# Kernel optimization log

Hardware: AMD Instinct MI355X
Metric: run time of the kernel (lower is better)

## Reference

```python
import jax, jax.numpy as jnp
import numpy as np

SHIFTS = (1, 2, 4, 8)
NL = 8  # num_layer: 8 fixed contrast kernels


def _base_kernels():
    d1 = np.array([[[-1, 0, 0], [0, 1, 0], [0, 0, 0]],
                   [[0, -1, 0], [0, 1, 0], [0, 0, 0]],
                   [[0, 0, -1], [0, 1, 0], [0, 0, 0]],
                   [[0, 0, 0], [0, 1, -1], [0, 0, 0]]], dtype=np.float32).reshape(4, 1, 3, 3)
    d2 = d1[:, :, ::-1, ::-1].copy()
    k = np.concatenate([d1, d2], axis=0)      # [8,1,3,3] fixed contrast kernels
    k0 = k.mean(0, keepdims=True)             # [1,1,3,3] mean kernel (kernel0)
    return jnp.asarray(k), jnp.asarray(k0)


def _depthwise(x, w, dilation):
    # x: [B,C,H,W], w: [C,1,3,3]; torch conv2d(padding='same', groups=C, dilation=d)
    return jax.lax.conv_general_dilated(
        x, w, window_strides=(1, 1), padding='SAME',
        rhs_dilation=(dilation, dilation),
        dimension_numbers=('NCHW', 'OIHW', 'NCHW'),
        feature_group_count=x.shape[1])


def _l2norm(x, eps=1e-12):
    # F.normalize(dim=-1): x / max(||x||_2, eps)
    n = jnp.sqrt(jnp.sum(x * x, axis=-1, keepdims=True))
    return x / jnp.maximum(n, eps)


def setup_inputs() -> dict:
    key = jax.random.key(0)
    ks = jax.random.split(key, 8)
    B, C, H, W = 8, 64, 96, 96
    nh = len(SHIFTS)
    hid = C // nh
    return {
        'cen': jax.random.normal(ks[0], (B, C, H, W), jnp.float32),
        'sum_weights': jax.random.normal(ks[1], (nh, C, 1, 1, 1, 2), jnp.float32),
        'q_w': jax.random.normal(ks[2], (nh, hid, C), jnp.float32) / np.sqrt(C),
        'k_w': jax.random.normal(ks[3], (nh, NL * hid, NL * C), jnp.float32) / np.sqrt(NL * C),
        'v_w': jax.random.normal(ks[4], (nh, NL * hid, NL * C), jnp.float32) / np.sqrt(NL * C),
        'out_w': jax.random.normal(ks[5], (C, C), jnp.float32) / np.sqrt(C),
        'bn_gamma': jnp.ones((C,), jnp.float32),
        'bn_beta': jnp.zeros((C,), jnp.float32),
    }


def reference(cen, sum_weights, q_w, k_w, v_w, out_w, bn_gamma, bn_beta):
    b, c, h, w = cen.shape
    nh = len(SHIFTS)
    K, K0 = _base_kernels()  # [8,1,3,3], [1,1,3,3]

    keys, qrys, vals = [], [], []
    for i, s in enumerate(SHIFTS):
        sw = jax.nn.softmax(sum_weights[i], axis=-1)  # [C,1,1,1,2]
        # mixed kernels: kernel_j*sw0 + kernel0*sw1 per channel -> [8,C,1,3,3]
        mixed = K[:, None] * sw[None, ..., 0] + K0[:, None] * sw[None, ..., 1]
        # 8 depthwise dilated convs, vmapped over the 8 kernels -> [8,B,C,H,W]
        surr = jax.vmap(lambda kw: _depthwise(cen, kw, s))(mixed)
        # torch.cat along channels in kernel-major order (j, c)
        surr = jnp.transpose(surr, (1, 0, 2, 3, 4)).reshape(b, NL * c, h, w)
        keys.append(jnp.einsum('oc,bchw->bohw', k_w[i], surr))
        vals.append(jnp.einsum('oc,bchw->bohw', v_w[i], surr))
        qrys.append(jnp.einsum('oc,bchw->bohw', q_w[i], cen))

    # torch: stack(dim=2).view(b, nh, -1, h*w)  (raw row-major reinterpret)
    keys = jnp.stack(keys, axis=2).reshape(b, nh, -1, h * w)
    qrys = jnp.stack(qrys, axis=2).reshape(b, nh, -1, h * w)
    vals = jnp.stack(vals, axis=2).reshape(b, nh, -1, h * w)

    k_n = _l2norm(keys)  # L2 norm over spatial axis
    q_n = _l2norm(qrys)
    # scores: [b, heads, hid, 8*hid]
    scores = jnp.einsum('bhqs,bhks->bhqk', q_n, k_n) / jnp.sqrt(jnp.float32(h * w))
    # InstanceNorm2d(num_heads), affine=False, eps=1e-5: per (b, head) over (q, k)
    mu = scores.mean(axis=(-2, -1), keepdims=True)
    var = scores.var(axis=(-2, -1), keepdims=True)
    attn = jax.nn.softmax((scores - mu) * jax.lax.rsqrt(var + 1e-5), axis=-1)
    out = jnp.einsum('bhqk,bhks->bhqs', attn, vals).reshape(b, c, h, w)

    # out_conv: 1x1 conv (no bias) + BatchNorm2d (train-mode batch stats) + ReLU
    y = jnp.einsum('oc,bchw->bohw', out_w, out)
    m = y.mean(axis=(0, 2, 3), keepdims=True)
    v2 = y.var(axis=(0, 2, 3), keepdims=True)
    y = (y - m) * jax.lax.rsqrt(v2 + 1e-5)
    y = y * bn_gamma[None, :, None, None] + bn_beta[None, :, None, None]
    return jax.nn.relu(y)
```

## Files before the change

### kernel.cpp

```cpp
#include <hip/hip_runtime.h>
#include <hip/hip_bf16.h>


#define WS_CEN    0UL
#define WS_SPART  12845056UL
#define WS_W      25690112UL
#define WS_Q      28049408UL
#define WS_KV     46923776UL
#define WS_KKP    197918720UL
#define WS_QQP    198213632UL
#define WS_ATTN   198250496UL
#define WS_AB     198512640UL
#define WS_BNP    217387008UL
#define WS_BNF    217681920UL

typedef __attribute__((ext_vector_type(8))) short short8;
typedef __attribute__((ext_vector_type(4))) float f32x4;

__device__ __forceinline__ float bflo(unsigned int u){ return __uint_as_float(u<<16); }
__device__ __forceinline__ float bfhi(unsigned int u){ return __uint_as_float(u & 0xffff0000u); }
__device__ __forceinline__ unsigned short f2bf(float f){
  unsigned int u = __float_as_uint(f);
  return (unsigned short)((u + 0x7fffu + ((u>>16)&1u)) >> 16);
}
__device__ __forceinline__ unsigned short fbits(float f){
  __hip_bfloat16 h = __float2bfloat16(f);
  return __builtin_bit_cast(unsigned short, h);
}

__global__ __launch_bounds__(256) void pad_kernel(const float* __restrict__ cen, unsigned short* __restrict__ cenbf){
  int idx = blockIdx.x*256 + threadIdx.x;
  int px = idx % 112; int t = idx / 112; int py = t % 112; int bc = t / 112;
  int y = py - 8, x = px - 8;
  float v = 0.f;
  if (y >= 0 && y < 96 && x >= 0 && x < 96) v = cen[(size_t)bc*9216 + y*96 + x];
  cenbf[idx] = fbits(v);
}

__global__ __launch_bounds__(256) void prep_kernel(const float* __restrict__ sumw,
    const float* __restrict__ kw, const float* __restrict__ vw, unsigned short* __restrict__ Wb){
  int idx = blockIdx.x*256 + threadIdx.x;
  int o = idx & 255; int r = idx >> 8; int c = r & 63; r >>= 6; int t = r % 9; int i = r / 9;
  float l0 = sumw[(i*64 + c)*2 + 0], l1 = sumw[(i*64 + c)*2 + 1];
  float m = fmaxf(l0, l1);
  float e0 = expf(l0 - m), e1 = expf(l1 - m);
  float inv = 1.f/(e0 + e1);
  float sw0 = e0*inv, sw1 = e1*inv;
  const float* wsrc = (o < 128) ? (kw + ((size_t)i*128 + o)*512 + c)
                                : (vw + ((size_t)i*128 + (o-128))*512 + c);
  float A = 0.f;
  #pragma unroll
  for (int j = 0; j < 8; ++j) A += wsrc[j*64];
  float val;
  if (t == 4) {
    val = A;
  } else {
    const int tmap[9] = {0,1,2,7,0,3,6,5,4};
    int j = tmap[t];
    val = -(wsrc[j*64]*sw0 + A*sw1*0.125f);
  }
  int k = t*64 + c;
  Wb[(((size_t)i*18 + (k>>5))*256 + o)*32 + (k&31)] = f2bf(val);
}

__global__ __launch_bounds__(256) void qproj_kernel(const float* __restrict__ cen,
    const float* __restrict__ qw, unsigned short* __restrict__ qbf){
  __shared__ float WT[64][64];
  int tid = threadIdx.x;
  int st = blockIdx.x, b = blockIdx.y;
  #pragma unroll
  for (int e = 0; e < 16; ++e) {
    int f = e*256 + tid; int c = f >> 6, row = f & 63;
    int i = row & 3, o = row >> 2;
    WT[c][row] = qw[(size_t)i*1024 + o*64 + c];
  }
  __syncthreads();
  int s = st*256 + tid;
  float acc[64];
  #pragma unroll
  for (int r = 0; r < 64; ++r) acc[r] = 0.f;
  const float* cb = cen + (size_t)b*64*9216 + s;
  for (int c = 0; c < 64; ++c) {
    float xv = cb[(size_t)c*9216];
    #pragma unroll
    for (int r4 = 0; r4 < 16; ++r4) {
      float4 w = *(const float4*)&WT[c][r4*4];
      acc[r4*4+0] = fmaf(w.x, xv, acc[r4*4+0]);
      acc[r4*4+1] = fmaf(w.y, xv, acc[r4*4+1]);
      acc[r4*4+2] = fmaf(w.z, xv, acc[r4*4+2]);
      acc[r4*4+3] = fmaf(w.w, xv, acc[r4*4+3]);
    }
  }
  unsigned short* qb = qbf + (size_t)b*64*9216 + s;
  #pragma unroll
  for (int r = 0; r < 64; ++r) qb[(size_t)r*9216] = fbits(acc[r]);
}

__global__ __launch_bounds__(256, 3) void conv_kv_mfma(const unsigned short* __restrict__ cenbf,
    const unsigned short* __restrict__ Wb, unsigned short* __restrict__ KV){
  __shared__ char Xs[2][128*72];
  const int tid = threadIdx.x;
  const int st = blockIdx.x, oc = blockIdx.y, ib = blockIdx.z;
  const int i = ib >> 3, b = ib & 7;
  const int dil = 1 << i;
  const int s0 = st*128;
  const int wave = tid >> 6, lane = tid & 63;
  const int wm = wave >> 1, wn = wave & 1;
  const int l15 = lane & 15, l4 = lane >> 4;
  const int s_idx = tid & 127;
  const int khalf = tid >> 7;
  const int s = s0 + s_idx;
  const int y = s / 96, x = s - y*96;
  const unsigned short* cb = cenbf + (size_t)b*802816 + (size_t)(y+8)*112 + (x+8);

  f32x4 acc[4][4];
  #pragma unroll
  for (int mf = 0; mf < 4; ++mf)
    #pragma unroll
    for (int nf = 0; nf < 4; ++nf)
      acc[mf][nf] = (f32x4){0.f, 0.f, 0.f, 0.f};

  const unsigned short* Wi = Wb + (size_t)i*18*8192;
  const unsigned short* apb = Wi + (size_t)(oc*128 + wm*64 + l15)*32 + l4*8;

  unsigned short vs[16];
  auto gather = [&](int kn){
    int t = kn >> 1;
    int cbase = (kn & 1)*32 + khalf*16;
    int dy = (t/3 - 1)*dil, dx = (t - (t/3)*3 - 1)*dil;
    const unsigned short* p = cb + (size_t)cbase*12544 + (dy*112 + dx);
    #pragma unroll
    for (int j = 0; j < 16; ++j) vs[j] = p[(size_t)j*12544];
  };

  gather(0);
  int buf = 0;
  for (int kc = 0; kc < 18; ++kc) {
    short8 a[4];
    const unsigned short* ap = apb + (size_t)kc*8192;
    #pragma unroll
    for (int mf = 0; mf < 4; ++mf) a[mf] = *(const short8*)(ap + mf*512);
    asm volatile("" ::: "memory");
    char* wp = Xs[buf] + s_idx*72 + khalf*32;
    #pragma unroll
    for (int w = 0; w < 4; ++w) {
      unsigned int p0 = (unsigned int)vs[4*w+0] | ((unsigned int)vs[4*w+1] << 16);
      unsigned int p1 = (unsigned int)vs[4*w+2] | ((unsigned int)vs[4*w+3] << 16);
      *(uint2*)(wp + w*8) = make_uint2(p0, p1);
    }
    if (kc < 17) gather(kc + 1);
    asm volatile("s_waitcnt lgkmcnt(0)" ::: "memory");
    __builtin_amdgcn_s_barrier();
    asm volatile("" ::: "memory");
    short8 bfr[4];
    #pragma unroll
    for (int nf = 0; nf < 4; ++nf) {
      const char* rp = Xs[buf] + (wn*64 + nf*16 + l15)*72 + l4*16;
      uint2 lo = *(const uint2*)rp;
      uint2 hi = *(const uint2*)(rp + 8);
      uint4 tb = make_uint4(lo.x, lo.y, hi.x, hi.y);
      bfr[nf] = *(short8*)&tb;
    }
    #pragma unroll
    for (int mf = 0; mf < 4; ++mf)
      #pragma unroll
      for (int nf = 0; nf < 4; ++nf)
        acc[mf][nf] = __builtin_amdgcn_mfma_f32_16x16x32_bf16(a[mf], bfr[nf], acc[mf][nf], 0, 0, 0);
    buf ^= 1;
  }

  #pragma unroll
  for (int mf = 0; mf < 4; ++mf) {
    #pragma unroll
    for (int nf = 0; nf < 4; ++nf) {
      int scol = s0 + wn*64 + nf*16 + l15;
      int obase = oc*128 + wm*64 + mf*16 + l4*4;
      #pragma unroll
      for (int r = 0; r < 4; ++r)
        KV[((size_t)ib*256 + obase + r)*9216 + scol] = fbits(acc[mf][nf][r]);
    }
  }
}

__global__ __launch_bounds__(256) void scores_mfma(const unsigned short* __restrict__ KV,
    const unsigned short* __restrict__ qbf, float* __restrict__ spart,
    float* __restrict__ kkpart, float* __restrict__ qqpart){
  __shared__ float red[4][2192];
  const int tid = threadIdx.x;
  const int chunk = blockIdx.x, hh = blockIdx.y, b = blockIdx.z;
  const int wave = tid >> 6, lane = tid & 63;
  const int l15 = lane & 15, l4 = lane >> 4;
  const int sbase = chunk*512 + wave*128;

  const unsigned short* qp = qbf + ((size_t)(b*64 + hh*16 + l15))*9216 + sbase + l4*8;
  const unsigned short* kp = KV + ((size_t)(((l15&3)*8 + b)*256 + hh*32 + (l15>>2)))*9216 + sbase + l4*8;

  f32x4 sacc[8], kkacc[8], qqacc;
  #pragma unroll
  for (int nf = 0; nf < 8; ++nf) { sacc[nf] = (f32x4){0,0,0,0}; kkacc[nf] = (f32x4){0,0,0,0}; }
  qqacc = (f32x4){0,0,0,0};

  #pragma unroll
  for (int sl = 0; sl < 4; ++sl) {
    short8 qf = *(const short8*)(qp + sl*32);
    short8 kf[8];
    #pragma unroll
    for (int nf = 0; nf < 8; ++nf) kf[nf] = *(const short8*)(kp + (size_t)nf*36864 + sl*32);
    qqacc = __builtin_amdgcn_mfma_f32_16x16x32_bf16(qf, qf, qqacc, 0, 0, 0);
    #pragma unroll
    for (int nf = 0; nf < 8; ++nf) {
      sacc[nf]  = __builtin_amdgcn_mfma_f32_16x16x32_bf16(qf, kf[nf], sacc[nf], 0, 0, 0);
      kkacc[nf] = __builtin_amdgcn_mfma_f32_16x16x32_bf16(kf[nf], kf[nf], kkacc[nf], 0, 0, 0);
    }
  }
  float* rw = red[wave];
  #pragma unroll
  for (int nf = 0; nf < 8; ++nf)
    #pragma unroll
    for (int r = 0; r < 4; ++r)
      rw[(l4*4 + r)*128 + nf*16 + l15] = sacc[nf][r];
  if ((l15 >> 2) == l4) {
    int r = l15 & 3;
    #pragma unroll
    for (int nf = 0; nf < 8; ++nf) rw[2048 + nf*16 + l15] = kkacc[nf][r];
    rw[2176 + l15] = qqacc[r];
  }
  __syncthreads();
  int pb = (b*4 + hh)*18 + chunk;
  for (int t = tid; t < 2192; t += 256) {
    float v = red[0][t] + red[1][t] + red[2][t] + red[3][t];
    if (t < 2048)       spart[(size_t)pb*2048 + t] = v;
    else if (t < 2176)  kkpart[(size_t)pb*128 + (t - 2048)] = v;
    else                qqpart[(size_t)pb*16 + (t - 2176)] = v;
  }
}

__global__ __launch_bounds__(256) void softmax_kernel(const float* __restrict__ spart,
    const float* __restrict__ kkpart, const float* __restrict__ qqpart, float* __restrict__ attnT){
  const int pb = blockIdx.x, tid = threadIdx.x;
  const int qr = tid >> 4, g = tid & 15;
  __shared__ float kkl[128];
  __shared__ float qql[16];
  __shared__ float red[8];
  __shared__ float stats[2];
  float sv[8] = {0,0,0,0,0,0,0,0};
  for (int ch = 0; ch < 18; ++ch) {
    const float* p = spart + ((size_t)(pb*18 + ch))*2048 + qr*128 + g*8;
    #pragma unroll
    for (int e = 0; e < 8; ++e) sv[e] += p[e];
  }
  if (tid < 128) { float ssum = 0.f; for (int ch = 0; ch < 18; ++ch) ssum += kkpart[(size_t)(pb*18+ch)*128 + tid]; kkl[tid] = ssum; }
  if (tid < 16)  { float ssum = 0.f; for (int ch = 0; ch < 18; ++ch) ssum += qqpart[(size_t)(pb*18+ch)*16 + tid]; qql[tid] = ssum; }
  __syncthreads();
  float qn = fmaxf(sqrtf(qql[qr]), 1e-12f);
  float lsum = 0.f, lsq = 0.f;
  #pragma unroll
  for (int e = 0; e < 8; ++e) {
    float kn = fmaxf(sqrtf(kkl[g*8+e]), 1e-12f);
    float v = sv[e] / (qn * kn * 96.0f);
    sv[e] = v; lsum += v; lsq += v*v;
  }
  #pragma unroll
  for (int m = 1; m <= 32; m <<= 1) { lsum += __shfl_xor(lsum, m); lsq += __shfl_xor(lsq, m); }
  if ((tid & 63) == 0) { red[tid >> 6] = lsum; red[4 + (tid >> 6)] = lsq; }
  __syncthreads();
  if (tid == 0) {
    float ts = red[0]+red[1]+red[2]+red[3];
    float tq = red[4]+red[5]+red[6]+red[7];
    float mean = ts / 2048.0f;
    float var = tq / 2048.0f - mean*mean;
    stats[0] = mean; stats[1] = rsqrtf(var + 1e-5f);
  }
  __syncthreads();
  float mean = stats[0], inv = stats[1];
  float mx = -1e30f;
  #pragma unroll
  for (int e = 0; e < 8; ++e) { sv[e] = (sv[e] - mean) * inv; mx = fmaxf(mx, sv[e]); }
  #pragma unroll
  for (int m = 1; m <= 8; m <<= 1) mx = fmaxf(mx, __shfl_xor(mx, m));
  float es = 0.f;
  #pragma unroll
  for (int e = 0; e < 8; ++e) { sv[e] = expf(sv[e] - mx); es += sv[e]; }
  #pragma unroll
  for (int m = 1; m <= 8; m <<= 1) es += __shfl_xor(es, m);
  float rinv = 1.0f / es;
  #pragma unroll
  for (int e = 0; e < 8; ++e) attnT[(size_t)pb*2048 + (g*8+e)*16 + qr] = sv[e] * rinv;
}

__global__ __launch_bounds__(256) void attnfold_kernel(const float* __restrict__ attnT,
    const float* __restrict__ ow, unsigned short* __restrict__ Ab){
  int idx = blockIdx.x*256 + threadIdx.x;
  int kr = idx & 127, hh = (idx >> 7) & 3, o2 = (idx >> 9) & 63, b = idx >> 15;
  const float* ap = attnT + ((size_t)(b*4 + hh))*2048 + kr*16;
  const float* wp = ow + o2*64 + hh*16;
  float acc = 0.f;
  #pragma unroll
  for (int qr = 0; qr < 16; ++qr) acc += wp[qr] * ap[qr];
  int rc = (kr & 3)*4 + hh, ch = kr >> 2;
  Ab[(((size_t)b*16 + rc)*64 + o2)*32 + ch] = fbits(acc);
}

__global__ __launch_bounds__(256, 3) void ygemm_kernel(const unsigned short* __restrict__ KV,
    const unsigned short* __restrict__ Ab, float* __restrict__ dout, float* __restrict__ bnpart){
  __shared__ char Xs[2][128*72];
  __shared__ float bns[4][32], bnq[4][32];
  const int tid = threadIdx.x;
  const int st = blockIdx.x, b = blockIdx.y;
  const int wave = tid >> 6, lane = tid & 63;
  const int wm = wave >> 1, wn = wave & 1;
  const int l15 = lane & 15, l4 = lane >> 4;
  const int s_idx = tid & 127, khalf = tid >> 7;
  const int s0 = st*128;

  f32x4 acc[2][4];
  #pragma unroll
  for (int mf = 0; mf < 2; ++mf)
    #pragma unroll
    for (int nf = 0; nf < 4; ++nf)
      acc[mf][nf] = (f32x4){0.f, 0.f, 0.f, 0.f};

  const unsigned short* Abb = Ab + ((size_t)b*16*64)*32 + (size_t)(wm*32 + l15)*32 + l4*8;

  unsigned short vs[16];
  auto vgather = [&](int kn){
    int vr = (((kn >> 2)*8 + b)*256 + 128 + (kn & 3)*32) + khalf*16;
    const unsigned short* p = KV + (size_t)vr*9216 + s0 + s_idx;
    #pragma unroll
    for (int j = 0; j < 16; ++j) vs[j] = p[(size_t)j*9216];
  };

  vgather(0);
  int buf = 0;
  for (int kc = 0; kc < 16; ++kc) {
    short8 a[2];
    #pragma unroll
    for (int mf = 0; mf < 2; ++mf) a[mf] = *(const short8*)(Abb + (size_t)kc*2048 + mf*512);
    asm volatile("" ::: "memory");
    char* wp = Xs[buf] + s_idx*72 + khalf*32;
    #pragma unroll
    for (int w = 0; w < 4; ++w) {
      unsigned int p0 = (unsigned int)vs[4*w+0] | ((unsigned int)vs[4*w+1] << 16);
      unsigned int p1 = (unsigned int)vs[4*w+2] | ((unsigned int)vs[4*w+3] << 16);
      *(uint2*)(wp + w*8) = make_uint2(p0, p1);
    }
    if (kc < 15) vgather(kc + 1);
    asm volatile("s_waitcnt lgkmcnt(0)" ::: "memory");
    __builtin_amdgcn_s_barrier();
    asm volatile("" ::: "memory");
    short8 bfr[4];
    #pragma unroll
    for (int nf = 0; nf < 4; ++nf) {
      const char* rp = Xs[buf] + (wn*64 + nf*16 + l15)*72 + l4*16;
      uint2 lo = *(const uint2*)rp;
      uint2 hi = *(const uint2*)(rp + 8);
      uint4 tb = make_uint4(lo.x, lo.y, hi.x, hi.y);
      bfr[nf] = *(short8*)&tb;
    }
    #pragma unroll
    for (int mf = 0; mf < 2; ++mf)
      #pragma unroll
      for (int nf = 0; nf < 4; ++nf)
        acc[mf][nf] = __builtin_amdgcn_mfma_f32_16x16x32_bf16(a[mf], bfr[nf], acc[mf][nf], 0, 0, 0);
    buf ^= 1;
  }

  #pragma unroll
  for (int mf = 0; mf < 2; ++mf) {
    #pragma unroll
    for (int rr = 0; rr < 4; ++rr) {
      int o2 = wm*32 + mf*16 + l4*4 + rr;
      float vsum = 0.f, vsq = 0.f;
      #pragma unroll
      for (int nf = 0; nf < 4; ++nf) {
        float v = acc[mf][nf][rr];
        vsum += v; vsq += v*v;
        dout[((size_t)(b*64 + o2))*9216 + s0 + wn*64 + nf*16 + l15] = v;
      }
      #pragma unroll
      for (int m = 1; m <= 8; m <<= 1) { vsum += __shfl_xor(vsum, m); vsq += __shfl_xor(vsq, m); }
      if (l15 == 0) { bns[wave][mf*16 + l4*4 + rr] = vsum; bnq[wave][mf*16 + l4*4 + rr] = vsq; }
    }
  }
  __syncthreads();
  if (tid < 64) {
    int wmq = tid >> 5, local = tid & 31;
    float s_ = bns[wmq*2][local] + bns[wmq*2+1][local];
    float q_ = bnq[wmq*2][local] + bnq[wmq*2+1][local];
    int bid = b*72 + st;
    bnpart[(size_t)bid*128 + tid] = s_;
    bnpart[(size_t)bid*128 + 64 + tid] = q_;
  }
}

__global__ __launch_bounds__(128) void bncombine_kernel(const float* __restrict__ bnpart, float* __restrict__ bnfin){
  int t = threadIdx.x;
  float a = 0.f;
  for (int blk = 0; blk < 576; ++blk) a += bnpart[(size_t)blk*128 + t];
  bnfin[t] = a;
}

__global__ __launch_bounds__(256) void bnapply_kernel(float* __restrict__ yb,
    const float* __restrict__ bnfin, const float* __restrict__ gamma, const float* __restrict__ beta){
  int gid = blockIdx.x*256 + threadIdx.x;
  int o = (gid / 2304) & 63;
  float mean = bnfin[o] * (1.f/73728.f);
  float var = bnfin[64 + o] * (1.f/73728.f) - mean*mean;
  float inv = rsqrtf(var + 1e-5f);
  float g = gamma[o], be = beta[o];
  float4 v = ((const float4*)yb)[gid];
  v.x = fmaxf((v.x - mean)*inv*g + be, 0.f);
  v.y = fmaxf((v.y - mean)*inv*g + be, 0.f);
  v.z = fmaxf((v.z - mean)*inv*g + be, 0.f);
  v.w = fmaxf((v.w - mean)*inv*g + be, 0.f);
  ((float4*)yb)[gid] = v;
}

extern "C" void kernel_launch(void* const* d_in, const int* in_sizes, int n_in,
                              void* d_out, int out_size, void* d_ws, size_t ws_size,
                              hipStream_t stream) {
  const float* cen   = (const float*)d_in[0];
  const float* sumw  = (const float*)d_in[1];
  const float* qw    = (const float*)d_in[2];
  const float* kw    = (const float*)d_in[3];
  const float* vw    = (const float*)d_in[4];
  const float* ow    = (const float*)d_in[5];
  const float* gamma = (const float*)d_in[6];
  const float* beta  = (const float*)d_in[7];

  char* ws = (char*)d_ws;
  unsigned short* cenbf  = (unsigned short*)(ws + WS_CEN);
  float*          spart  = (float*)(ws + WS_SPART);
  unsigned short* Wb     = (unsigned short*)(ws + WS_W);
  unsigned short* qbf    = (unsigned short*)(ws + WS_Q);
  unsigned short* KV     = (unsigned short*)(ws + WS_KV);
  float*          kkp    = (float*)(ws + WS_KKP);
  float*          qqp    = (float*)(ws + WS_QQP);
  float*          attnT  = (float*)(ws + WS_ATTN);
  unsigned short* Ab     = (unsigned short*)(ws + WS_AB);
  float*          bnp    = (float*)(ws + WS_BNP);
  float*          bnf    = (float*)(ws + WS_BNF);

  pad_kernel     <<<25088, 256, 0, stream>>>(cen, cenbf);
  prep_kernel    <<<2304, 256, 0, stream>>>(sumw, kw, vw, Wb);
  qproj_kernel   <<<dim3(36, 8), 256, 0, stream>>>(cen, qw, qbf);
  conv_kv_mfma   <<<dim3(72, 2, 32), 256, 0, stream>>>(cenbf, Wb, KV);
  scores_mfma    <<<dim3(18, 4, 8), 256, 0, stream>>>(KV, qbf, spart, kkp, qqp);
  softmax_kernel <<<32, 256, 0, stream>>>(spart, kkp, qqp, attnT);
  attnfold_kernel<<<1024, 256, 0, stream>>>(attnT, ow, Ab);
  ygemm_kernel   <<<dim3(72, 8), 256, 0, stream>>>(KV, Ab, (float*)d_out, bnp);
  bncombine_kernel<<<1, 128, 0, stream>>>(bnp, bnf);
  bnapply_kernel <<<4608, 256, 0, stream>>>((float*)d_out, bnf, gamma, beta);
}
```

Before: 427.7 us.

## Enlarge conv_kv tile to full 256 outputs and gather pixel pairs via shifted copy

The dilated-conv MFMA kernel now has each 512-thread block compute all 256 output channels for 256 spatial positions, so the input gather is no longer repeated across two output-channel blocks. Each thread loads two adjacent bf16 pixels with one 32-bit load. To keep those loads aligned for odd horizontal offsets, the pad kernel writes a second copy of the padded input shifted by one element. The weight layout is reorganised per tap with K=64 per step, and the workspace offsets are reshuffled to make room for the extra copy. The costs are more registers per thread (32 accumulator tiles, 16 A fragments), a larger LDS footprint, half as many blocks, and one extra padded-input write.

```diff
diff --git a/kernel.cpp b/kernel.cpp
--- a/kernel.cpp
+++ b/kernel.cpp
@@ -3,16 +3,17 @@
 
 
 #define WS_CEN    0UL
-#define WS_SPART  12845056UL
+#define WS_CEN1   12845056UL
 #define WS_W      25690112UL
 #define WS_Q      28049408UL
 #define WS_KV     46923776UL
-#define WS_KKP    197918720UL
-#define WS_QQP    198213632UL
-#define WS_ATTN   198250496UL
-#define WS_AB     198512640UL
-#define WS_BNP    217387008UL
-#define WS_BNF    217681920UL
+#define WS_SPART  197918720UL
+#define WS_KKP    202637312UL
+#define WS_QQP    202932224UL
+#define WS_ATTN   202969088UL
+#define WS_AB     203231232UL
+#define WS_BNP    203755520UL
+#define WS_BNF    204050432UL
 
 typedef __attribute__((ext_vector_type(8))) short short8;
 typedef __attribute__((ext_vector_type(4))) float f32x4;
@@ -28,13 +29,16 @@
   return __builtin_bit_cast(unsigned short, h);
 }
 
-__global__ __launch_bounds__(256) void pad_kernel(const float* __restrict__ cen, unsigned short* __restrict__ cenbf){
+__global__ __launch_bounds__(256) void pad_kernel(const float* __restrict__ cen,
+    unsigned short* __restrict__ cenbf, unsigned short* __restrict__ cenbf1){
   int idx = blockIdx.x*256 + threadIdx.x;
   int px = idx % 112; int t = idx / 112; int py = t % 112; int bc = t / 112;
   int y = py - 8, x = px - 8;
   float v = 0.f;
   if (y >= 0 && y < 96 && x >= 0 && x < 96) v = cen[(size_t)bc*9216 + y*96 + x];
-  cenbf[idx] = fbits(v);
+  unsigned short h = fbits(v);
+  cenbf[idx] = h;
+  if (idx > 0) cenbf1[idx-1] = h;
 }
 
 __global__ __launch_bounds__(256) void prep_kernel(const float* __restrict__ sumw,
@@ -59,8 +63,7 @@
     int j = tmap[t];
     val = -(wsrc[j*64]*sw0 + A*sw1*0.125f);
   }
-  int k = t*64 + c;
-  Wb[(((size_t)i*18 + (k>>5))*256 + o)*32 + (k&31)] = f2bf(val);
+  Wb[(((size_t)i*9 + t)*256 + o)*64 + c] = f2bf(val);
 }
 
 __global__ __launch_bounds__(256) void qproj_kernel(const float* __restrict__ cen,
@@ -96,85 +99,101 @@
   for (int r = 0; r < 64; ++r) qb[(size_t)r*9216] = fbits(acc[r]);
 }
 
-__global__ __launch_bounds__(256, 3) void conv_kv_mfma(const unsigned short* __restrict__ cenbf,
-    const unsigned short* __restrict__ Wb, unsigned short* __restrict__ KV){
-  __shared__ char Xs[2][128*72];
+__global__ __launch_bounds__(512, 2) void conv_kv_mfma(const unsigned short* __restrict__ cenbf,
+    const unsigned short* __restrict__ cenbf1, const unsigned short* __restrict__ Wb,
+    unsigned short* __restrict__ KV){
+  __shared__ char Xs[2][256*136];
   const int tid = threadIdx.x;
-  const int st = blockIdx.x, oc = blockIdx.y, ib = blockIdx.z;
+  const int st = blockIdx.x, ib = blockIdx.z;
   const int i = ib >> 3, b = ib & 7;
   const int dil = 1 << i;
-  const int s0 = st*128;
+  const int s0 = st*256;
   const int wave = tid >> 6, lane = tid & 63;
-  const int wm = wave >> 1, wn = wave & 1;
+  const int wm = wave >> 2, wn = wave & 3;
   const int l15 = lane & 15, l4 = lane >> 4;
-  const int s_idx = tid & 127;
-  const int khalf = tid >> 7;
-  const int s = s0 + s_idx;
+  const int p = tid & 127, cg = tid >> 7;
+  const int sl = 2*p;
+  const int s = s0 + sl;
   const int y = s / 96, x = s - y*96;
-  const unsigned short* cb = cenbf + (size_t)b*802816 + (size_t)(y+8)*112 + (x+8);
-
-  f32x4 acc[4][4];
-  #pragma unroll
-  for (int mf = 0; mf < 4; ++mf)
+  const long ebase = (long)b*802816 + (long)(cg*16)*12544 + (long)(y+8)*112 + (x+8);
+
+  f32x4 acc[8][4];
+  #pragma unroll
+  for (int mf = 0; mf < 8; ++mf)
     #pragma unroll
     for (int nf = 0; nf < 4; ++nf)
       acc[mf][nf] = (f32x4){0.f, 0.f, 0.f, 0.f};
 
-  const unsigned short* Wi = Wb + (size_t)i*18*8192;
-  const unsigned short* apb = Wi + (size_t)(oc*128 + wm*64 + l15)*32 + l4*8;
-
-  unsigned short vs[16];
-  auto gather = [&](int kn){
-    int t = kn >> 1;
-    int cbase = (kn & 1)*32 + khalf*16;
+  const unsigned short* Wi = Wb + (size_t)i*9*16384;
+  const unsigned short* apb = Wi + (size_t)(wm*128 + l15)*64 + l4*8;
+
+  unsigned int vs[16];
+  auto gather = [&](int t){
     int dy = (t/3 - 1)*dil, dx = (t - (t/3)*3 - 1)*dil;
-    const unsigned short* p = cb + (size_t)cbase*12544 + (dy*112 + dx);
-    #pragma unroll
-    for (int j = 0; j < 16; ++j) vs[j] = p[(size_t)j*12544];
+    long e0 = ebase + dy*112 + dx;
+    const unsigned short* src = (dx & 1) ? (cenbf1 + (e0 - 1)) : (cenbf + e0);
+    #pragma unroll
+    for (int j = 0; j < 16; ++j) vs[j] = *(const unsigned int*)(src + (size_t)j*12544);
   };
 
   gather(0);
   int buf = 0;
-  for (int kc = 0; kc < 18; ++kc) {
-    short8 a[4];
-    const unsigned short* ap = apb + (size_t)kc*8192;
-    #pragma unroll
-    for (int mf = 0; mf < 4; ++mf) a[mf] = *(const short8*)(ap + mf*512);
+  for (int t = 0; t < 9; ++t) {
+    short8 a[8][2];
+    const unsigned short* ap = apb + (size_t)t*16384;
+    #pragma unroll
+    for (int mf = 0; mf < 8; ++mf)
+      #pragma unroll
+      for (int ks = 0; ks < 2; ++ks)
+        a[mf][ks] = *(const short8*)(ap + mf*1024 + ks*32);
     asm volatile("" ::: "memory");
-    char* wp = Xs[buf] + s_idx*72 + khalf*32;
-    #pragma unroll
-    for (int w = 0; w < 4; ++w) {
-      unsigned int p0 = (unsigned int)vs[4*w+0] | ((unsigned int)vs[4*w+1] << 16);
-      unsigned int p1 = (unsigned int)vs[4*w+2] | ((unsigned int)vs[4*w+3] << 16);
-      *(uint2*)(wp + w*8) = make_uint2(p0, p1);
-    }
-    if (kc < 17) gather(kc + 1);
+    {
+      unsigned int lo[8], hi[8];
+      #pragma unroll
+      for (int w = 0; w < 8; ++w) {
+        lo[w] = (vs[2*w] & 0xffffu) | (vs[2*w+1] << 16);
+        hi[w] = (vs[2*w] >> 16)    | (vs[2*w+1] & 0xffff0000u);
+      }
+      char* r0 = Xs[buf] + sl*136 + cg*32;
+      char* r1 = r0 + 136;
+      #pragma unroll
+      for (int w = 0; w < 4; ++w) {
+        *(uint2*)(r0 + w*8) = make_uint2(lo[2*w], lo[2*w+1]);
+        *(uint2*)(r1 + w*8) = make_uint2(hi[2*w], hi[2*w+1]);
+      }
+    }
+    if (t < 8) gather(t + 1);
     asm volatile("s_waitcnt lgkmcnt(0)" ::: "memory");
     __builtin_amdgcn_s_barrier();
     asm volatile("" ::: "memory");
-    short8 bfr[4];
+    short8 bfr[4][2];
     #pragma unroll
     for (int nf = 0; nf < 4; ++nf) {
-      const char* rp = Xs[buf] + (wn*64 + nf*16 + l15)*72 + l4*16;
-      uint2 lo = *(const uint2*)rp;
-      uint2 hi = *(const uint2*)(rp + 8);
-      uint4 tb = make_uint4(lo.x, lo.y, hi.x, hi.y);
-      bfr[nf] = *(short8*)&tb;
-    }
-    #pragma unroll
-    for (int mf = 0; mf < 4; ++mf)
-      #pragma unroll
-      for (int nf = 0; nf < 4; ++nf)
-        acc[mf][nf] = __builtin_amdgcn_mfma_f32_16x16x32_bf16(a[mf], bfr[nf], acc[mf][nf], 0, 0, 0);
+      const char* rp = Xs[buf] + (wn*64 + nf*16 + l15)*136 + l4*16;
+      #pragma unroll
+      for (int ks = 0; ks < 2; ++ks) {
+        uint2 lo2 = *(const uint2*)(rp + ks*64);
+        uint2 hi2 = *(const uint2*)(rp + ks*64 + 8);
+        uint4 tb = make_uint4(lo2.x, lo2.y, hi2.x, hi2.y);
+        bfr[nf][ks] = *(short8*)&tb;
+      }
+    }
+    #pragma unroll
+    for (int ks = 0; ks < 2; ++ks)
+      #pragma unroll
+      for (int mf = 0; mf < 8; ++mf)
+        #pragma unroll
+        for (int nf = 0; nf < 4; ++nf)
+          acc[mf][nf] = __builtin_amdgcn_mfma_f32_16x16x32_bf16(a[mf][ks], bfr[nf][ks], acc[mf][nf], 0, 0, 0);
     buf ^= 1;
   }
 
   #pragma unroll
-  for (int mf = 0; mf < 4; ++mf) {
+  for (int mf = 0; mf < 8; ++mf) {
     #pragma unroll
     for (int nf = 0; nf < 4; ++nf) {
       int scol = s0 + wn*64 + nf*16 + l15;
-      int obase = oc*128 + wm*64 + mf*16 + l4*4;
+      int obase = wm*128 + mf*16 + l4*4;
       #pragma unroll
       for (int r = 0; r < 4; ++r)
         KV[((size_t)ib*256 + obase + r)*9216 + scol] = fbits(acc[mf][nf][r]);
@@ -430,10 +449,11 @@
 
   char* ws = (char*)d_ws;
   unsigned short* cenbf  = (unsigned short*)(ws + WS_CEN);
-  float*          spart  = (float*)(ws + WS_SPART);
+  unsigned short* cenbf1 = (unsigned short*)(ws + WS_CEN1);
   unsigned short* Wb     = (unsigned short*)(ws + WS_W);
   unsigned short* qbf    = (unsigned short*)(ws + WS_Q);
   unsigned short* KV     = (unsigned short*)(ws + WS_KV);
+  float*          spart  = (float*)(ws + WS_SPART);
   float*          kkp    = (float*)(ws + WS_KKP);
   float*          qqp    = (float*)(ws + WS_QQP);
   float*          attnT  = (float*)(ws + WS_ATTN);
@@ -441,10 +461,10 @@
   float*          bnp    = (float*)(ws + WS_BNP);
   float*          bnf    = (float*)(ws + WS_BNF);
 
-  pad_kernel     <<<25088, 256, 0, stream>>>(cen, cenbf);
+  pad_kernel     <<<25088, 256, 0, stream>>>(cen, cenbf, cenbf1);
   prep_kernel    <<<2304, 256, 0, stream>>>(sumw, kw, vw, Wb);
   qproj_kernel   <<<dim3(36, 8), 256, 0, stream>>>(cen, qw, qbf);
-  conv_kv_mfma   <<<dim3(72, 2, 32), 256, 0, stream>>>(cenbf, Wb, KV);
+  conv_kv_mfma   <<<dim3(36, 1, 32), 512, 0, stream>>>(cenbf, cenbf1, Wb, KV);
   scores_mfma    <<<dim3(18, 4, 8), 256, 0, stream>>>(KV, qbf, spart, kkp, qqp);
   softmax_kernel <<<32, 256, 0, stream>>>(spart, kkp, qqp, attnT);
   attnfold_kernel<<<1024, 256, 0, stream>>>(attnT, ow, Ab);
```

New measurement: 415.0 us. -3.0%, faster.

## Use channel-last padded bf16 input so conv loads B fragments directly

Applied to the files above, without the earlier changes.

Replaces the NCHW padded bf16 copy with a channel-last (NHWC) padded layout built via an LDS transpose plus a memset for the border. The KV conv kernel then loads each 16-byte B fragment straight from global memory, which removes the strided 16-way scalar gather, the LDS staging and the barriers. The spatial tile doubles to 256 per block with 8 N-fragments per wave. The larger accumulator lowers occupancy (launch bounds 2), and the dilated neighbour reads now rely on cache hits instead of LDS reuse.

```diff
diff --git a/kernel.cpp b/kernel.cpp
--- a/kernel.cpp
+++ b/kernel.cpp
@@ -3,16 +3,16 @@
 
 
 #define WS_CEN    0UL
-#define WS_SPART  12845056UL
 #define WS_W      25690112UL
 #define WS_Q      28049408UL
 #define WS_KV     46923776UL
-#define WS_KKP    197918720UL
-#define WS_QQP    198213632UL
-#define WS_ATTN   198250496UL
-#define WS_AB     198512640UL
-#define WS_BNP    217387008UL
-#define WS_BNF    217681920UL
+#define WS_SPART  197918720UL
+#define WS_KKP    202637312UL
+#define WS_QQP    202932224UL
+#define WS_ATTN   202969088UL
+#define WS_AB     203231232UL
+#define WS_BNP    203755520UL
+#define WS_BNF    204050432UL
 
 typedef __attribute__((ext_vector_type(8))) short short8;
 typedef __attribute__((ext_vector_type(4))) float f32x4;
@@ -28,13 +28,26 @@
   return __builtin_bit_cast(unsigned short, h);
 }
 
-__global__ __launch_bounds__(256) void pad_kernel(const float* __restrict__ cen, unsigned short* __restrict__ cenbf){
-  int idx = blockIdx.x*256 + threadIdx.x;
-  int px = idx % 112; int t = idx / 112; int py = t % 112; int bc = t / 112;
-  int y = py - 8, x = px - 8;
-  float v = 0.f;
-  if (y >= 0 && y < 96 && x >= 0 && x < 96) v = cen[(size_t)bc*9216 + y*96 + x];
-  cenbf[idx] = fbits(v);
+__global__ __launch_bounds__(256) void padT_kernel(const float* __restrict__ cen,
+    unsigned short* __restrict__ cenT){
+  __shared__ float T[64][97];
+  int y = blockIdx.x, b = blockIdx.y;
+  int tid = threadIdx.x;
+  const float* src = cen + (size_t)b*64*9216 + y*96;
+  #pragma unroll
+  for (int ch = 0; ch < 24; ++ch) {
+    int idx = ch*256 + tid;
+    int c = idx / 96, x = idx - c*96;
+    T[c][x] = src[(size_t)c*9216 + x];
+  }
+  __syncthreads();
+  unsigned short* dst = cenT + (((size_t)b*112 + y + 8)*112 + 8)*64;
+  #pragma unroll
+  for (int ch = 0; ch < 24; ++ch) {
+    int idx = ch*256 + tid;
+    int x = idx >> 6, c = idx & 63;
+    dst[(size_t)x*64 + c] = fbits(T[c][x]);
+  }
 }
 
 __global__ __launch_bounds__(256) void prep_kernel(const float* __restrict__ sumw,
@@ -96,84 +109,57 @@
   for (int r = 0; r < 64; ++r) qb[(size_t)r*9216] = fbits(acc[r]);
 }
 
-__global__ __launch_bounds__(256, 3) void conv_kv_mfma(const unsigned short* __restrict__ cenbf,
+__global__ __launch_bounds__(256, 2) void conv_kv_mfma(const unsigned short* __restrict__ cenT,
     const unsigned short* __restrict__ Wb, unsigned short* __restrict__ KV){
-  __shared__ char Xs[2][128*72];
   const int tid = threadIdx.x;
   const int st = blockIdx.x, oc = blockIdx.y, ib = blockIdx.z;
   const int i = ib >> 3, b = ib & 7;
   const int dil = 1 << i;
-  const int s0 = st*128;
+  const int s0 = st*256;
   const int wave = tid >> 6, lane = tid & 63;
   const int wm = wave >> 1, wn = wave & 1;
   const int l15 = lane & 15, l4 = lane >> 4;
-  const int s_idx = tid & 127;
-  const int khalf = tid >> 7;
-  const int s = s0 + s_idx;
-  const int y = s / 96, x = s - y*96;
-  const unsigned short* cb = cenbf + (size_t)b*802816 + (size_t)(y+8)*112 + (x+8);
-
-  f32x4 acc[4][4];
+
+  int offs[8];
+  #pragma unroll
+  for (int nf = 0; nf < 8; ++nf) {
+    int s = s0 + wn*128 + nf*16 + l15;
+    int y = s / 96, x = s - y*96;
+    offs[nf] = ((y+8)*112 + (x+8))*64 + l4*8;
+  }
+  const unsigned short* cb = cenT + (size_t)b*802816;
+  const unsigned short* apb = Wb + (size_t)i*147456 + (size_t)(oc*128 + wm*64 + l15)*32 + l4*8;
+
+  f32x4 acc[4][8];
   #pragma unroll
   for (int mf = 0; mf < 4; ++mf)
     #pragma unroll
-    for (int nf = 0; nf < 4; ++nf)
+    for (int nf = 0; nf < 8; ++nf)
       acc[mf][nf] = (f32x4){0.f, 0.f, 0.f, 0.f};
 
-  const unsigned short* Wi = Wb + (size_t)i*18*8192;
-  const unsigned short* apb = Wi + (size_t)(oc*128 + wm*64 + l15)*32 + l4*8;
-
-  unsigned short vs[16];
-  auto gather = [&](int kn){
-    int t = kn >> 1;
-    int cbase = (kn & 1)*32 + khalf*16;
+  for (int kc = 0; kc < 18; ++kc) {
+    int t = kc >> 1;
     int dy = (t/3 - 1)*dil, dx = (t - (t/3)*3 - 1)*dil;
-    const unsigned short* p = cb + (size_t)cbase*12544 + (dy*112 + dx);
-    #pragma unroll
-    for (int j = 0; j < 16; ++j) vs[j] = p[(size_t)j*12544];
-  };
-
-  gather(0);
-  int buf = 0;
-  for (int kc = 0; kc < 18; ++kc) {
+    int duni = (dy*112 + dx)*64 + (kc & 1)*32;
     short8 a[4];
     const unsigned short* ap = apb + (size_t)kc*8192;
     #pragma unroll
     for (int mf = 0; mf < 4; ++mf) a[mf] = *(const short8*)(ap + mf*512);
-    asm volatile("" ::: "memory");
-    char* wp = Xs[buf] + s_idx*72 + khalf*32;
-    #pragma unroll
-    for (int w = 0; w < 4; ++w) {
-      unsigned int p0 = (unsigned int)vs[4*w+0] | ((unsigned int)vs[4*w+1] << 16);
-      unsigned int p1 = (unsigned int)vs[4*w+2] | ((unsigned int)vs[4*w+3] << 16);
-      *(uint2*)(wp + w*8) = make_uint2(p0, p1);
-    }
-    if (kc < 17) gather(kc + 1);
-    asm volatile("s_waitcnt lgkmcnt(0)" ::: "memory");
-    __builtin_amdgcn_s_barrier();
-    asm volatile("" ::: "memory");
-    short8 bfr[4];
-    #pragma unroll
-    for (int nf = 0; nf < 4; ++nf) {
-      const char* rp = Xs[buf] + (wn*64 + nf*16 + l15)*72 + l4*16;
-      uint2 lo = *(const uint2*)rp;
-      uint2 hi = *(const uint2*)(rp + 8);
-      uint4 tb = make_uint4(lo.x, lo.y, hi.x, hi.y);
-      bfr[nf] = *(short8*)&tb;
-    }
+    short8 bf[8];
+    #pragma unroll
+    for (int nf = 0; nf < 8; ++nf) bf[nf] = *(const short8*)(cb + offs[nf] + duni);
     #pragma unroll
     for (int mf = 0; mf < 4; ++mf)
       #pragma unroll
-      for (int nf = 0; nf < 4; ++nf)
-        acc[mf][nf] = __builtin_amdgcn_mfma_f32_16x16x32_bf16(a[mf], bfr[nf], acc[mf][nf], 0, 0, 0);
-    buf ^= 1;
+      for (int nf = 0; nf < 8; ++nf)
+        acc[mf][nf] = __builtin_amdgcn_mfma_f32_16x16x32_bf16(a[mf], bf[nf], acc[mf][nf], 0, 0, 0);
   }
 
   #pragma unroll
   for (int mf = 0; mf < 4; ++mf) {
     #pragma unroll
-    for (int nf = 0; nf < 4; ++nf) {
-      int scol = s0 + wn*64 + nf*16 + l15;
+    for (int nf = 0; nf < 8; ++nf) {
+      int scol = s0 + wn*128 + nf*16 + l15;
       int obase = oc*128 + wm*64 + mf*16 + l4*4;
       #pragma unroll
       for (int r = 0; r < 4; ++r)
@@ -429,11 +415,11 @@
   const float* beta  = (const float*)d_in[7];
 
   char* ws = (char*)d_ws;
-  unsigned short* cenbf  = (unsigned short*)(ws + WS_CEN);
-  float*          spart  = (float*)(ws + WS_SPART);
+  unsigned short* cenT   = (unsigned short*)(ws + WS_CEN);
   unsigned short* Wb     = (unsigned short*)(ws + WS_W);
   unsigned short* qbf    = (unsigned short*)(ws + WS_Q);
   unsigned short* KV     = (unsigned short*)(ws + WS_KV);
+  float*          spart  = (float*)(ws + WS_SPART);
   float*          kkp    = (float*)(ws + WS_KKP);
   float*          qqp    = (float*)(ws + WS_QQP);
   float*          attnT  = (float*)(ws + WS_ATTN);
@@ -441,10 +427,11 @@
   float*          bnp    = (float*)(ws + WS_BNP);
   float*          bnf    = (float*)(ws + WS_BNF);
 
-  pad_kernel     <<<25088, 256, 0, stream>>>(cen, cenbf);
+  hipMemsetAsync(cenT, 0, 12845056UL, stream);
+  padT_kernel    <<<dim3(96, 8), 256, 0, stream>>>(cen, cenT);
   prep_kernel    <<<2304, 256, 0, stream>>>(sumw, kw, vw, Wb);
   qproj_kernel   <<<dim3(36, 8), 256, 0, stream>>>(cen, qw, qbf);
-  conv_kv_mfma   <<<dim3(72, 2, 32), 256, 0, stream>>>(cenbf, Wb, KV);
+  conv_kv_mfma   <<<dim3(36, 2, 32), 256, 0, stream>>>(cenT, Wb, KV);
   scores_mfma    <<<dim3(18, 4, 8), 256, 0, stream>>>(KV, qbf, spart, kkp, qqp);
   softmax_kernel <<<32, 256, 0, stream>>>(spart, kkp, qqp, attnT);
   attnfold_kernel<<<1024, 256, 0, stream>>>(attnT, ow, Ab);
```

Measured after the change: 428.2 us. No clear change (+0.1%).
